# Kernel optimization log

Measured on AMD Instinct MI355X. Metric: run time of the kernel, lower is better.

The kernel has to match this reference:

```python
import jax, jax.numpy as jnp
import numpy as np

N_NODES = 50000
N_EDGES = 800000
N_GRAPHS = 64
D_IN, D_HID, D_OUT = 128, 64, 32


def setup_inputs() -> dict:
    key = jax.random.key(0)
    ks = jax.random.split(key, 5)
    x = jax.random.normal(ks[0], (N_NODES, D_IN), dtype=jnp.float32)
    edge_index = jax.random.randint(ks[1], (2, N_EDGES), 0, N_NODES, dtype=jnp.int64)
    batch = jnp.sort(jax.random.randint(ks[2], (N_NODES,), 0, N_GRAPHS, dtype=jnp.int64))
    W1 = jax.random.normal(ks[3], (D_IN, D_HID), dtype=jnp.float32) * (1.0 / np.sqrt(D_IN))
    b1 = jnp.zeros((D_HID,), dtype=jnp.float32)
    W2 = jax.random.normal(ks[4], (D_HID, D_OUT), dtype=jnp.float32) * (1.0 / np.sqrt(D_HID))
    b2 = jnp.zeros((D_OUT,), dtype=jnp.float32)
    return {"x": x, "edge_index": edge_index, "batch": batch,
            "W1": W1, "b1": b1, "W2": W2, "b2": b2}


def gcn_conv(x, W, b, src, dst, num_nodes):
    # GCNConv with self-loops and symmetric normalization:
    # out = D^{-1/2} (A+I) D^{-1/2} X W + b
    loop = jnp.arange(num_nodes, dtype=src.dtype)
    s = jnp.concatenate([src, loop])
    d = jnp.concatenate([dst, loop])
    deg = jax.ops.segment_sum(jnp.ones_like(d, dtype=x.dtype), d, num_segments=num_nodes)
    dinv = jnp.where(deg > 0, jax.lax.rsqrt(deg), 0.0)
    h = x @ W                                   # [N, d_out]
    norm = (dinv[s] * dinv[d])[:, None]          # [E+N, 1]
    msg = h[s] * norm                            # gather + scale
    out = jax.ops.segment_sum(msg, d, num_segments=num_nodes)  # scatter-add
    return out + b


def reference(x, edge_index, batch, W1, b1, W2, b2):
    # T.NormalizeFeatures(): row-normalize features (sum clamped to >= 1)
    x = x / jnp.clip(jnp.sum(x, axis=-1, keepdims=True), 1.0, None)
    src, dst = edge_index[0], edge_index[1]
    h = jax.nn.relu(gcn_conv(x, W1, b1, src, dst, N_NODES))
    h = jax.nn.relu(gcn_conv(h, W2, b2, src, dst, N_NODES))
    # global mean pool over graphs
    sums = jax.ops.segment_sum(h, batch, num_segments=N_GRAPHS)
    counts = jax.ops.segment_sum(jnp.ones((N_NODES,), h.dtype), batch, num_segments=N_GRAPHS)
    return sums / jnp.clip(counts, 1.0, None)[:, None]
```

## Files before the change

### kernel.cpp

```cpp
#include <hip/hip_runtime.h>

#define N_NODES 50000
#define N_EDGES 800000
#define N_GRAPHS 64
#define D_IN 128
#define D_HID 64
#define D_OUT 32
#define POOL_TILE 512
#define G1_NT 8
#define NPART ((N_NODES + 255) >> 8)
#define BSTRIDE 5120
#define EPB 4096

typedef __attribute__((ext_vector_type(8))) short bf16x8;
typedef __attribute__((ext_vector_type(4))) float f32x4;

__device__ __forceinline__ unsigned short bf16r(float f) {
    unsigned int u = __float_as_uint(f);
    return (unsigned short)((u + 0x7fffu + ((u >> 16) & 1u)) >> 16);
}
__device__ __forceinline__ float2 bf2(unsigned int w) {
    return make_float2(__uint_as_float(w << 16), __uint_as_float(w & 0xffff0000u));
}

__global__ __launch_bounds__(256) void k_init(const float* __restrict__ W1,
                                              unsigned short* __restrict__ wph,
                                              unsigned short* __restrict__ wpl,
                                              float* __restrict__ psum,
                                              int* __restrict__ bin_cursor) {
    for (int i = threadIdx.x; i < N_GRAPHS * D_OUT; i += 256) psum[i] = 0.0f;
    for (int i = threadIdx.x; i < NPART; i += 256) bin_cursor[i] = 0;
    for (int idx = threadIdx.x; idx < D_IN * D_HID; idx += 256) {
        int k = idx >> 6, c = idx & 63;
        float w = W1[idx];
        unsigned int b = __float_as_uint(w);
        unsigned short h = (unsigned short)(b >> 16);
        float fh = __uint_as_float(b & 0xffff0000u);
        unsigned short l = (unsigned short)(__float_as_uint(w - fh) >> 16);
        int kt = k >> 5, oct = (k >> 3) & 3, i = k & 7;
        int nt = c >> 4, col = c & 15;
        int dst = ((kt * 4 + nt) * 64 + (oct * 16 + col)) * 8 + i;
        wph[dst] = h;
        wpl[dst] = l;
    }
}

__global__ __launch_bounds__(256) void k_binA(const int* __restrict__ src,
                                              const int* __restrict__ dst,
                                              int* __restrict__ bin_cursor,
                                              unsigned int* __restrict__ binbuf) {
    __shared__ int cnt[NPART];
    __shared__ int boff[NPART];
    __shared__ int gbase[NPART];
    __shared__ int tmp[256];
    __shared__ unsigned int stage[EPB];

    const int tid = threadIdx.x;
    const int e0 = blockIdx.x * EPB;
    const int nvalid = min(EPB, N_EDGES - e0);

    for (int i = tid; i < NPART; i += 256) cnt[i] = 0;
    __syncthreads();

    unsigned int ee[16];
    const int i40 = e0 >> 2;
    #pragma unroll
    for (int j = 0; j < 4; ++j) {
        int i4 = i40 + j * 256 + tid;
        if (4 * i4 + 3 < N_EDGES) {
            int4 s4 = ((const int4*)src)[i4];
            int4 d4 = ((const int4*)dst)[i4];
            ee[4*j+0] = (unsigned)(s4.x | ((d4.x & 255) << 16) | ((d4.x >> 8) << 24));
            ee[4*j+1] = (unsigned)(s4.y | ((d4.y & 255) << 16) | ((d4.y >> 8) << 24));
            ee[4*j+2] = (unsigned)(s4.z | ((d4.z & 255) << 16) | ((d4.z >> 8) << 24));
            ee[4*j+3] = (unsigned)(s4.w | ((d4.w & 255) << 16) | ((d4.w >> 8) << 24));
        } else {
            #pragma unroll
            for (int k = 0; k < 4; ++k) {
                int e = 4 * i4 + k;
                if (e < N_EDGES) {
                    int s = src[e], d = dst[e];
                    ee[4*j+k] = (unsigned)(s | ((d & 255) << 16) | ((d >> 8) << 24));
                } else {
                    ee[4*j+k] = 0xFFFFFFFFu;
                }
            }
        }
    }

    #pragma unroll
    for (int j = 0; j < 16; ++j) {
        unsigned int p = ee[j] >> 24;
        if (p < NPART) atomicAdd(&cnt[p], 1);
    }
    __syncthreads();

    tmp[tid] = (tid < NPART) ? cnt[tid] : 0;
    __syncthreads();
    for (int off = 1; off < 256; off <<= 1) {
        int t = (tid >= off) ? tmp[tid - off] : 0;
        __syncthreads();
        tmp[tid] += t;
        __syncthreads();
    }
    if (tid < NPART) {
        int c = cnt[tid];
        int b = tmp[tid] - c;
        boff[tid] = b;
        gbase[tid] = atomicAdd(&bin_cursor[tid], c);
        cnt[tid] = b;
    }
    __syncthreads();

    #pragma unroll
    for (int j = 0; j < 16; ++j) {
        unsigned int p = ee[j] >> 24;
        if (p < NPART) {
            int lp = atomicAdd(&cnt[p], 1);
            stage[lp] = ee[j];
        }
    }
    __syncthreads();

    for (int j = tid; j < nvalid; j += 256) {
        unsigned int e = stage[j];
        int p = e >> 24;
        binbuf[(size_t)p * BSTRIDE + gbase[p] + (j - boff[p])] = e;
    }
}

__global__ __launch_bounds__(256) void k_csr(const int* __restrict__ bin_cursor,
                                             const unsigned int* __restrict__ binbuf,
                                             int* __restrict__ rowptr,
                                             float* __restrict__ dinv,
                                             int* __restrict__ csr_src) {
    __shared__ int sh[256];
    const int p = blockIdx.x, tid = threadIdx.x;

    sh[tid] = (tid < p) ? bin_cursor[tid] : 0;
    __syncthreads();
    for (int off = 128; off; off >>= 1) {
        if (tid < off) sh[tid] += sh[tid + off];
        __syncthreads();
    }
    const int offset = sh[0];
    __syncthreads();

    sh[tid] = 0;
    __syncthreads();
    const unsigned int* b = binbuf + (size_t)p * BSTRIDE;
    const int n = bin_cursor[p];
    for (int j = tid; j < n; j += 256) atomicAdd(&sh[(b[j] >> 16) & 255], 1);
    __syncthreads();
    const int deg = sh[tid];
    __syncthreads();

    sh[tid] = deg;
    __syncthreads();
    for (int off = 1; off < 256; off <<= 1) {
        int t = (tid >= off) ? sh[tid - off] : 0;
        __syncthreads();
        sh[tid] += t;
        __syncthreads();
    }
    const int rp = offset + sh[tid] - deg;
    const int node = p * 256 + tid;
    if (node < N_NODES) {
        rowptr[node] = rp;
        dinv[node] = rsqrtf((float)(deg + 1));
    }
    if (node == N_NODES) rowptr[N_NODES] = N_EDGES;
    __syncthreads();

    sh[tid] = rp;
    __syncthreads();
    for (int j = tid; j < n; j += 256) {
        unsigned int e = b[j];
        int pos = atomicAdd(&sh[(e >> 16) & 255], 1);
        csr_src[pos] = (int)(e & 0xFFFFu);
    }
}

__global__ __launch_bounds__(256) void k_mm1(const float* __restrict__ x,
                                             const unsigned short* __restrict__ wph,
                                             const unsigned short* __restrict__ wpl,
                                             const float* __restrict__ dinv,
                                             unsigned short* __restrict__ hs1b) {
    const int lane = threadIdx.x & 63;
    const int gw = blockIdx.x * 4 + (threadIdx.x >> 6);
    const int node0 = gw * 16;
    if (node0 >= N_NODES) return;
    const int r16 = lane & 15, oct = lane >> 4;
    const int rowAc = min(node0 + r16, N_NODES - 1);

    const float* xr = x + (size_t)rowAc * D_IN + oct * 32;
    float rs = 0.f;
    #pragma unroll
    for (int q = 0; q < 8; ++q) {
        float4 v = ((const float4*)xr)[q];
        rs += (v.x + v.y) + (v.z + v.w);
    }
    rs += __shfl_xor(rs, 16, 64);
    rs += __shfl_xor(rs, 32, 64);
    const float ls = (1.0f / fmaxf(rs, 1.0f)) * dinv[rowAc];

    f32x4 acc[4] = {};
    #pragma unroll
    for (int kt = 0; kt < 4; ++kt) {
        const float* ap = x + (size_t)rowAc * D_IN + kt * 32 + oct * 8;
        float4 a0 = ((const float4*)ap)[0];
        float4 a1 = ((const float4*)ap)[1];
        float f[8] = {a0.x, a0.y, a0.z, a0.w, a1.x, a1.y, a1.z, a1.w};
        bf16x8 ahi, alo;
        #pragma unroll
        for (int j = 0; j < 8; ++j) {
            float fs = f[j] * ls;
            unsigned int b = __float_as_uint(fs);
            ahi[j] = (short)(b >> 16);
            float fh = __uint_as_float(b & 0xffff0000u);
            alo[j] = (short)(__float_as_uint(fs - fh) >> 16);
        }
        #pragma unroll
        for (int nt = 0; nt < 4; ++nt) {
            int fo = ((kt * 4 + nt) * 64 + lane) * 8;
            bf16x8 bh = *(const bf16x8*)(wph + fo);
            bf16x8 bl = *(const bf16x8*)(wpl + fo);
            acc[nt] = __builtin_amdgcn_mfma_f32_16x16x32_bf16(ahi, bh, acc[nt], 0, 0, 0);
            acc[nt] = __builtin_amdgcn_mfma_f32_16x16x32_bf16(ahi, bl, acc[nt], 0, 0, 0);
            acc[nt] = __builtin_amdgcn_mfma_f32_16x16x32_bf16(alo, bh, acc[nt], 0, 0, 0);
        }
    }
    #pragma unroll
    for (int nt = 0; nt < 4; ++nt) {
        #pragma unroll
        for (int r = 0; r < 4; ++r) {
            int node = node0 + oct * 4 + r;
            if (node < N_NODES)
                hs1b[(size_t)node * D_HID + nt * 16 + r16] = bf16r(acc[nt][r]);
        }
    }
}

__global__ __launch_bounds__(256) void k_g1m2(const int* __restrict__ rowptr,
                                              const int* __restrict__ csr_src,
                                              const unsigned short* __restrict__ hs1b,
                                              const float* __restrict__ dinv,
                                              const float* __restrict__ b1,
                                              const float* __restrict__ W2,
                                              unsigned short* __restrict__ hs2b) {
    const int lane = threadIdx.x & 63;
    const int g = lane >> 4;
    const int q = lane & 15;
    const int c = lane & 31;
    const int kh = lane >> 5;

    float w2r[32];
    #pragma unroll
    for (int j = 0; j < 32; ++j) w2r[j] = W2[(kh * 32 + j) * D_OUT + c];
    const f32x4 bb = ((const f32x4*)b1)[q];

    const int node0 = (blockIdx.x * 4 + (threadIdx.x >> 6)) * G1_NT;

    for (int t = 0; t < G1_NT; ++t) {
        const int v = node0 + t;
        if (v >= N_NODES) break;

        const int beg = rowptr[v], end = rowptr[v + 1];
        f32x4 a0 = {0,0,0,0}, a1 = {0,0,0,0}, a2 = {0,0,0,0}, a3 = {0,0,0,0};
        if (g == 0) {
            uint2 w = ((const uint2*)(hs1b + (size_t)v * D_HID))[q];
            float2 t0 = bf2(w.x), t1 = bf2(w.y);
            a0[0] += t0.x; a0[1] += t0.y; a0[2] += t1.x; a0[3] += t1.y;
        }

        int e = beg + g;
        for (; e + 12 < end; e += 16) {
            int s0 = csr_src[e];
            int s1 = csr_src[e + 4];
            int s2 = csr_src[e + 8];
            int s3 = csr_src[e + 12];
            uint2 w0 = ((const uint2*)(hs1b + (size_t)s0 * D_HID))[q];
            uint2 w1 = ((const uint2*)(hs1b + (size_t)s1 * D_HID))[q];
            uint2 w2 = ((const uint2*)(hs1b + (size_t)s2 * D_HID))[q];
            uint2 w3 = ((const uint2*)(hs1b + (size_t)s3 * D_HID))[q];
            float2 t0, t1;
            t0 = bf2(w0.x); t1 = bf2(w0.y);
            a0[0] += t0.x; a0[1] += t0.y; a0[2] += t1.x; a0[3] += t1.y;
            t0 = bf2(w1.x); t1 = bf2(w1.y);
            a1[0] += t0.x; a1[1] += t0.y; a1[2] += t1.x; a1[3] += t1.y;
            t0 = bf2(w2.x); t1 = bf2(w2.y);
            a2[0] += t0.x; a2[1] += t0.y; a2[2] += t1.x; a2[3] += t1.y;
            t0 = bf2(w3.x); t1 = bf2(w3.y);
            a3[0] += t0.x; a3[1] += t0.y; a3[2] += t1.x; a3[3] += t1.y;
        }
        for (; e < end; e += 4) {
            int s0 = csr_src[e];
            uint2 w0 = ((const uint2*)(hs1b + (size_t)s0 * D_HID))[q];
            float2 t0 = bf2(w0.x), t1 = bf2(w0.y);
            a0[0] += t0.x; a0[1] += t0.y; a0[2] += t1.x; a0[3] += t1.y;
        }
        f32x4 acc = (a0 + a1) + (a2 + a3);

        #pragma unroll
        for (int m = 16; m <= 32; m <<= 1) {
            f32x4 o;
            o[0] = __shfl_xor(acc[0], m, 64);
            o[1] = __shfl_xor(acc[1], m, 64);
            o[2] = __shfl_xor(acc[2], m, 64);
            o[3] = __shfl_xor(acc[3], m, 64);
            acc += o;
        }

        const float dv = dinv[v];
        f32x4 h;
        #pragma unroll
        for (int j = 0; j < 4; ++j) h[j] = fmaxf(dv * acc[j] + bb[j], 0.0f);

        float a = 0.0f;
        #pragma unroll
        for (int qq = 0; qq < 8; ++qq) {
            const int Q = kh * 8 + qq;
            a += __shfl(h[0], Q, 64) * w2r[4 * qq + 0];
            a += __shfl(h[1], Q, 64) * w2r[4 * qq + 1];
            a += __shfl(h[2], Q, 64) * w2r[4 * qq + 2];
            a += __shfl(h[3], Q, 64) * w2r[4 * qq + 3];
        }
        a += __shfl_xor(a, 32, 64);
        if (kh == 0) hs2b[(size_t)v * D_OUT + c] = bf16r(a * dv);
    }
}

__global__ __launch_bounds__(256) void k_gather2(const int* __restrict__ rowptr,
                                                 const int* __restrict__ csr_src,
                                                 const unsigned short* __restrict__ hs2b,
                                                 const float* __restrict__ dinv,
                                                 const float* __restrict__ b2,
                                                 float* __restrict__ p) {
    int v = blockIdx.x * 4 + (threadIdx.x >> 6);
    if (v >= N_NODES) return;
    const int lane = threadIdx.x & 63;
    const int g = lane >> 3;
    const int q = lane & 7;

    const int beg = rowptr[v], end = rowptr[v + 1];
    f32x4 a0 = {0,0,0,0}, a1 = {0,0,0,0};
    if (g == 0) {
        uint2 w = ((const uint2*)(hs2b + (size_t)v * D_OUT))[q];
        float2 t0 = bf2(w.x), t1 = bf2(w.y);
        a0[0] += t0.x; a0[1] += t0.y; a0[2] += t1.x; a0[3] += t1.y;
    }

    int e = beg + g;
    for (; e + 8 < end; e += 16) {
        int s0 = csr_src[e];
        int s1 = csr_src[e + 8];
        uint2 w0 = ((const uint2*)(hs2b + (size_t)s0 * D_OUT))[q];
        uint2 w1 = ((const uint2*)(hs2b + (size_t)s1 * D_OUT))[q];
        float2 t0, t1;
        t0 = bf2(w0.x); t1 = bf2(w0.y);
        a0[0] += t0.x; a0[1] += t0.y; a0[2] += t1.x; a0[3] += t1.y;
        t0 = bf2(w1.x); t1 = bf2(w1.y);
        a1[0] += t0.x; a1[1] += t0.y; a1[2] += t1.x; a1[3] += t1.y;
    }
    if (e < end) {
        int s0 = csr_src[e];
        uint2 w0 = ((const uint2*)(hs2b + (size_t)s0 * D_OUT))[q];
        float2 t0 = bf2(w0.x), t1 = bf2(w0.y);
        a0[0] += t0.x; a0[1] += t0.y; a0[2] += t1.x; a0[3] += t1.y;
    }
    f32x4 acc = a0 + a1;

    #pragma unroll
    for (int m = 8; m <= 32; m <<= 1) {
        f32x4 o;
        o[0] = __shfl_xor(acc[0], m, 64);
        o[1] = __shfl_xor(acc[1], m, 64);
        o[2] = __shfl_xor(acc[2], m, 64);
        o[3] = __shfl_xor(acc[3], m, 64);
        acc += o;
    }

    if (g == 0) {
        const float dv = dinv[v];
        f32x4 bb = ((const f32x4*)b2)[q];
        f32x4 r;
        #pragma unroll
        for (int j = 0; j < 4; ++j) r[j] = fmaxf(dv * acc[j] + bb[j], 0.0f);
        ((f32x4*)(p + (size_t)v * D_OUT))[q] = r;
    }
}

__global__ __launch_bounds__(256) void k_pool(const float* __restrict__ p,
                                              const int* __restrict__ batch,
                                              float* __restrict__ psum) {
    const int c = threadIdx.x & 31;
    const int slot = threadIdx.x >> 5;
    const int base = blockIdx.x * POOL_TILE;

    float acc = 0.0f;
    int curg = -1;
    for (int j = slot; j < POOL_TILE; j += 8) {
        int node = base + j;
        if (node >= N_NODES) break;
        float hv = p[(size_t)node * D_OUT + c];
        int g = batch[node];
        if (g != curg) {
            if (curg >= 0) atomicAdd(&psum[curg * D_OUT + c], acc);
            curg = g;
            acc = 0.0f;
        }
        acc += hv;
    }
    if (curg >= 0) atomicAdd(&psum[curg * D_OUT + c], acc);
}

__global__ __launch_bounds__(256) void k_final(const float* __restrict__ psum,
                                               const int* __restrict__ batch,
                                               float* __restrict__ out) {
    int i = blockIdx.x * 256 + threadIdx.x;
    if (i < N_GRAPHS * D_OUT) {
        int g = i >> 5;
        int lo = 0, hi = N_NODES;
        while (lo < hi) { int m = (lo + hi) >> 1; if (batch[m] < g) lo = m + 1; else hi = m; }
        int lb = lo;
        lo = 0; hi = N_NODES;
        while (lo < hi) { int m = (lo + hi) >> 1; if (batch[m] <= g) lo = m + 1; else hi = m; }
        float cnt = (float)(lo - lb);
        out[i] = psum[i] / fmaxf(cnt, 1.0f);
    }
}

extern "C" void kernel_launch(void* const* d_in, const int* in_sizes, int n_in,
                              void* d_out, int out_size, void* d_ws, size_t ws_size,
                              hipStream_t stream) {
    const float* x     = (const float*)d_in[0];
    const int*   edge  = (const int*)d_in[1];
    const int*   batch = (const int*)d_in[2];
    const float* W1    = (const float*)d_in[3];
    const float* b1    = (const float*)d_in[4];
    const float* W2    = (const float*)d_in[5];
    const float* b2    = (const float*)d_in[6];
    float* out = (float*)d_out;

    const int* src = edge;
    const int* dst = edge + N_EDGES;

    float* ws   = (float*)d_ws;
    float* dinv = ws;
    unsigned short* hs1b = (unsigned short*)(dinv + N_NODES);
    unsigned short* hs2b = hs1b + (size_t)N_NODES * D_HID;
    float* p    = (float*)(hs2b + (size_t)N_NODES * D_OUT);
    float* psum = p + (size_t)N_NODES * D_OUT;
    int* bin_cursor = (int*)(psum + N_GRAPHS * D_OUT);
    int* rowptr  = bin_cursor + NPART;
    int* csr_src = rowptr + N_NODES + 1;
    unsigned int* binbuf = (unsigned int*)(csr_src + N_EDGES);
    unsigned short* wph = (unsigned short*)(binbuf + (size_t)NPART * BSTRIDE);
    unsigned short* wpl = wph + D_IN * D_HID;

    k_init   <<<1, 256, 0, stream>>>(W1, wph, wpl, psum, bin_cursor);
    k_binA   <<<(N_EDGES + EPB - 1) / EPB, 256, 0, stream>>>(src, dst, bin_cursor, binbuf);
    k_csr    <<<NPART, 256, 0, stream>>>(bin_cursor, binbuf, rowptr, dinv, csr_src);
    k_mm1    <<<(N_NODES + 63) / 64, 256, 0, stream>>>(x, wph, wpl, dinv, hs1b);
    k_g1m2   <<<(N_NODES + 4 * G1_NT - 1) / (4 * G1_NT), 256, 0, stream>>>(rowptr, csr_src, hs1b, dinv, b1, W2, hs2b);
    k_gather2<<<(N_NODES + 3) / 4, 256, 0, stream>>>(rowptr, csr_src, hs2b, dinv, b2, p);
    k_pool   <<<(N_NODES + POOL_TILE - 1) / POOL_TILE, 256, 0, stream>>>(p, batch, psum);
    k_final  <<<(N_GRAPHS * D_OUT + 255) / 256, 256, 0, stream>>>(psum, batch, out);
}
```

Before: 155.5 us.

## Software-pipeline neighbor row gathers across consecutive nodes in both aggregation kernels

Both gather kernels now prefetch the first few neighbor indices and feature rows of the next node while the current node is being reduced, shuffled and written. The goal is to hide global-memory gather latency. The second gather kernel also changes from one node per wave to eight consecutive nodes per wave, so it launches far fewer blocks. The prefetch reads csr_src speculatively past the end of each row and masks indices to 16 bits to keep the addresses in range. This relies on the node count fitting in 16 bits and adds register pressure.

```diff
diff --git a/kernel.cpp b/kernel.cpp
--- a/kernel.cpp
+++ b/kernel.cpp
@@ -8,6 +8,9 @@
 #define D_OUT 32
 #define POOL_TILE 512
 #define G1_NT 8
+#define G2_NT 8
+#define PF1 8
+#define PF2 4
 #define NPART ((N_NODES + 255) >> 8)
 #define BSTRIDE 5120
 #define EPB 4096
@@ -260,46 +263,60 @@
     const f32x4 bb = ((const f32x4*)b1)[q];
 
     const int node0 = (blockIdx.x * 4 + (threadIdx.x >> 6)) * G1_NT;
+    if (node0 >= N_NODES) return;
+
+    int begC = rowptr[node0];
+    int endC = rowptr[node0 + 1];
+    int idxP[PF1];
+    #pragma unroll
+    for (int i = 0; i < PF1; ++i) idxP[i] = csr_src[begC + g + 4 * i] & 0xFFFF;
+    uint2 rowsC[PF1];
+    #pragma unroll
+    for (int i = 0; i < PF1; ++i)
+        rowsC[i] = ((const uint2*)(hs1b + (size_t)idxP[i] * D_HID))[q];
 
     for (int t = 0; t < G1_NT; ++t) {
         const int v = node0 + t;
         if (v >= N_NODES) break;
-
-        const int beg = rowptr[v], end = rowptr[v + 1];
-        f32x4 a0 = {0,0,0,0}, a1 = {0,0,0,0}, a2 = {0,0,0,0}, a3 = {0,0,0,0};
+        const bool haveNext = (t < G1_NT - 1) && (v + 1 < N_NODES);
+
+        const int begN = endC;
+        int endN = endC;
+        int idxN[PF1];
+        if (haveNext) {
+            endN = rowptr[v + 2];
+            #pragma unroll
+            for (int i = 0; i < PF1; ++i) idxN[i] = csr_src[begN + g + 4 * i] & 0xFFFF;
+        }
+
+        f32x4 acc0 = {0,0,0,0}, acc1 = {0,0,0,0};
         if (g == 0) {
             uint2 w = ((const uint2*)(hs1b + (size_t)v * D_HID))[q];
             float2 t0 = bf2(w.x), t1 = bf2(w.y);
-            a0[0] += t0.x; a0[1] += t0.y; a0[2] += t1.x; a0[3] += t1.y;
-        }
-
-        int e = beg + g;
-        for (; e + 12 < end; e += 16) {
-            int s0 = csr_src[e];
-            int s1 = csr_src[e + 4];
-            int s2 = csr_src[e + 8];
-            int s3 = csr_src[e + 12];
-            uint2 w0 = ((const uint2*)(hs1b + (size_t)s0 * D_HID))[q];
-            uint2 w1 = ((const uint2*)(hs1b + (size_t)s1 * D_HID))[q];
-            uint2 w2 = ((const uint2*)(hs1b + (size_t)s2 * D_HID))[q];
-            uint2 w3 = ((const uint2*)(hs1b + (size_t)s3 * D_HID))[q];
-            float2 t0, t1;
-            t0 = bf2(w0.x); t1 = bf2(w0.y);
-            a0[0] += t0.x; a0[1] += t0.y; a0[2] += t1.x; a0[3] += t1.y;
-            t0 = bf2(w1.x); t1 = bf2(w1.y);
-            a1[0] += t0.x; a1[1] += t0.y; a1[2] += t1.x; a1[3] += t1.y;
-            t0 = bf2(w2.x); t1 = bf2(w2.y);
-            a2[0] += t0.x; a2[1] += t0.y; a2[2] += t1.x; a2[3] += t1.y;
-            t0 = bf2(w3.x); t1 = bf2(w3.y);
-            a3[0] += t0.x; a3[1] += t0.y; a3[2] += t1.x; a3[3] += t1.y;
-        }
-        for (; e < end; e += 4) {
-            int s0 = csr_src[e];
-            uint2 w0 = ((const uint2*)(hs1b + (size_t)s0 * D_HID))[q];
-            float2 t0 = bf2(w0.x), t1 = bf2(w0.y);
-            a0[0] += t0.x; a0[1] += t0.y; a0[2] += t1.x; a0[3] += t1.y;
-        }
-        f32x4 acc = (a0 + a1) + (a2 + a3);
+            acc0[0] += t0.x; acc0[1] += t0.y; acc0[2] += t1.x; acc0[3] += t1.y;
+        }
+        #pragma unroll
+        for (int i = 0; i < PF1; ++i) {
+            if (begC + g + 4 * i < endC) {
+                float2 t0 = bf2(rowsC[i].x), t1 = bf2(rowsC[i].y);
+                if (i & 1) { acc1[0]+=t0.x; acc1[1]+=t0.y; acc1[2]+=t1.x; acc1[3]+=t1.y; }
+                else       { acc0[0]+=t0.x; acc0[1]+=t0.y; acc0[2]+=t1.x; acc0[3]+=t1.y; }
+            }
+        }
+        for (int e = begC + g + 4 * PF1; e < endC; e += 4) {
+            int s = csr_src[e];
+            uint2 w = ((const uint2*)(hs1b + (size_t)s * D_HID))[q];
+            float2 t0 = bf2(w.x), t1 = bf2(w.y);
+            acc0[0]+=t0.x; acc0[1]+=t0.y; acc0[2]+=t1.x; acc0[3]+=t1.y;
+        }
+        f32x4 acc = acc0 + acc1;
+
+        uint2 rowsN[PF1];
+        if (haveNext) {
+            #pragma unroll
+            for (int i = 0; i < PF1; ++i)
+                rowsN[i] = ((const uint2*)(hs1b + (size_t)idxN[i] * D_HID))[q];
+        }
 
         #pragma unroll
         for (int m = 16; m <= 32; m <<= 1) {
@@ -327,6 +344,12 @@
         }
         a += __shfl_xor(a, 32, 64);
         if (kh == 0) hs2b[(size_t)v * D_OUT + c] = bf16r(a * dv);
+
+        if (haveNext) {
+            begC = begN; endC = endN;
+            #pragma unroll
+            for (int i = 0; i < PF1; ++i) rowsC[i] = rowsN[i];
+        }
     }
 }
 
@@ -336,57 +359,88 @@
                                                  const float* __restrict__ dinv,
                                                  const float* __restrict__ b2,
                                                  float* __restrict__ p) {
-    int v = blockIdx.x * 4 + (threadIdx.x >> 6);
-    if (v >= N_NODES) return;
     const int lane = threadIdx.x & 63;
     const int g = lane >> 3;
     const int q = lane & 7;
 
-    const int beg = rowptr[v], end = rowptr[v + 1];
-    f32x4 a0 = {0,0,0,0}, a1 = {0,0,0,0};
-    if (g == 0) {
-        uint2 w = ((const uint2*)(hs2b + (size_t)v * D_OUT))[q];
-        float2 t0 = bf2(w.x), t1 = bf2(w.y);
-        a0[0] += t0.x; a0[1] += t0.y; a0[2] += t1.x; a0[3] += t1.y;
-    }
-
-    int e = beg + g;
-    for (; e + 8 < end; e += 16) {
-        int s0 = csr_src[e];
-        int s1 = csr_src[e + 8];
-        uint2 w0 = ((const uint2*)(hs2b + (size_t)s0 * D_OUT))[q];
-        uint2 w1 = ((const uint2*)(hs2b + (size_t)s1 * D_OUT))[q];
-        float2 t0, t1;
-        t0 = bf2(w0.x); t1 = bf2(w0.y);
-        a0[0] += t0.x; a0[1] += t0.y; a0[2] += t1.x; a0[3] += t1.y;
-        t0 = bf2(w1.x); t1 = bf2(w1.y);
-        a1[0] += t0.x; a1[1] += t0.y; a1[2] += t1.x; a1[3] += t1.y;
-    }
-    if (e < end) {
-        int s0 = csr_src[e];
-        uint2 w0 = ((const uint2*)(hs2b + (size_t)s0 * D_OUT))[q];
-        float2 t0 = bf2(w0.x), t1 = bf2(w0.y);
-        a0[0] += t0.x; a0[1] += t0.y; a0[2] += t1.x; a0[3] += t1.y;
-    }
-    f32x4 acc = a0 + a1;
-
-    #pragma unroll
-    for (int m = 8; m <= 32; m <<= 1) {
-        f32x4 o;
-        o[0] = __shfl_xor(acc[0], m, 64);
-        o[1] = __shfl_xor(acc[1], m, 64);
-        o[2] = __shfl_xor(acc[2], m, 64);
-        o[3] = __shfl_xor(acc[3], m, 64);
-        acc += o;
-    }
-
-    if (g == 0) {
-        const float dv = dinv[v];
-        f32x4 bb = ((const f32x4*)b2)[q];
-        f32x4 r;
-        #pragma unroll
-        for (int j = 0; j < 4; ++j) r[j] = fmaxf(dv * acc[j] + bb[j], 0.0f);
-        ((f32x4*)(p + (size_t)v * D_OUT))[q] = r;
+    const int node0 = (blockIdx.x * 4 + (threadIdx.x >> 6)) * G2_NT;
+    if (node0 >= N_NODES) return;
+    const f32x4 bb = ((const f32x4*)b2)[q];
+
+    int begC = rowptr[node0];
+    int endC = rowptr[node0 + 1];
+    int idxP[PF2];
+    #pragma unroll
+    for (int i = 0; i < PF2; ++i) idxP[i] = csr_src[begC + g + 8 * i] & 0xFFFF;
+    uint2 rowsC[PF2];
+    #pragma unroll
+    for (int i = 0; i < PF2; ++i)
+        rowsC[i] = ((const uint2*)(hs2b + (size_t)idxP[i] * D_OUT))[q];
+
+    for (int t = 0; t < G2_NT; ++t) {
+        const int v = node0 + t;
+        if (v >= N_NODES) break;
+        const bool haveNext = (t < G2_NT - 1) && (v + 1 < N_NODES);
+
+        const int begN = endC;
+        int endN = endC;
+        int idxN[PF2];
+        if (haveNext) {
+            endN = rowptr[v + 2];
+            #pragma unroll
+            for (int i = 0; i < PF2; ++i) idxN[i] = csr_src[begN + g + 8 * i] & 0xFFFF;
+        }
+
+        f32x4 acc = {0,0,0,0};
+        if (g == 0) {
+            uint2 w = ((const uint2*)(hs2b + (size_t)v * D_OUT))[q];
+            float2 t0 = bf2(w.x), t1 = bf2(w.y);
+            acc[0] += t0.x; acc[1] += t0.y; acc[2] += t1.x; acc[3] += t1.y;
+        }
+        #pragma unroll
+        for (int i = 0; i < PF2; ++i) {
+            if (begC + g + 8 * i < endC) {
+                float2 t0 = bf2(rowsC[i].x), t1 = bf2(rowsC[i].y);
+                acc[0] += t0.x; acc[1] += t0.y; acc[2] += t1.x; acc[3] += t1.y;
+            }
+        }
+        for (int e = begC + g + 8 * PF2; e < endC; e += 8) {
+            int s = csr_src[e];
+            uint2 w = ((const uint2*)(hs2b + (size_t)s * D_OUT))[q];
+            float2 t0 = bf2(w.x), t1 = bf2(w.y);
+            acc[0] += t0.x; acc[1] += t0.y; acc[2] += t1.x; acc[3] += t1.y;
+        }
+
+        uint2 rowsN[PF2];
+        if (haveNext) {
+            #pragma unroll
+            for (int i = 0; i < PF2; ++i)
+                rowsN[i] = ((const uint2*)(hs2b + (size_t)idxN[i] * D_OUT))[q];
+        }
+
+        #pragma unroll
+        for (int m = 8; m <= 32; m <<= 1) {
+            f32x4 o;
+            o[0] = __shfl_xor(acc[0], m, 64);
+            o[1] = __shfl_xor(acc[1], m, 64);
+            o[2] = __shfl_xor(acc[2], m, 64);
+            o[3] = __shfl_xor(acc[3], m, 64);
+            acc += o;
+        }
+
+        if (g == 0) {
+            const float dv = dinv[v];
+            f32x4 r;
+            #pragma unroll
+            for (int j = 0; j < 4; ++j) r[j] = fmaxf(dv * acc[j] + bb[j], 0.0f);
+            ((f32x4*)(p + (size_t)v * D_OUT))[q] = r;
+        }
+
+        if (haveNext) {
+            begC = begN; endC = endN;
+            #pragma unroll
+            for (int i = 0; i < PF2; ++i) rowsC[i] = rowsN[i];
+        }
     }
 }
 
@@ -463,7 +517,7 @@
     k_csr    <<<NPART, 256, 0, stream>>>(bin_cursor, binbuf, rowptr, dinv, csr_src);
     k_mm1    <<<(N_NODES + 63) / 64, 256, 0, stream>>>(x, wph, wpl, dinv, hs1b);
     k_g1m2   <<<(N_NODES + 4 * G1_NT - 1) / (4 * G1_NT), 256, 0, stream>>>(rowptr, csr_src, hs1b, dinv, b1, W2, hs2b);
-    k_gather2<<<(N_NODES + 3) / 4, 256, 0, stream>>>(rowptr, csr_src, hs2b, dinv, b2, p);
+    k_gather2<<<(N_NODES + 4 * G2_NT - 1) / (4 * G2_NT), 256, 0, stream>>>(rowptr, csr_src, hs2b, dinv, b2, p);
     k_pool   <<<(N_NODES + POOL_TILE - 1) / POOL_TILE, 256, 0, stream>>>(p, batch, psum);
     k_final  <<<(N_GRAPHS * D_OUT + 255) / 256, 256, 0, stream>>>(psum, batch, out);
 }
```

Measured after the change: 140.0 us. -10.0%, faster.
